# Performance work log

Hardware: AMD Instinct MI355X
Metric: run time of the kernel (lower is better)

The kernel has to match this reference:

```python
import jax, jax.numpy as jnp
import numpy as np

NEG = -1e30  # log-domain 'zero' (safe stand-in for -inf)


def _ctc_loss(logits, labels, label_length, logit_length):
    """Dense-label CTC loss, blank = last class, logits [B,T,C] batch-major.

    Matches tf.nn.ctc_loss(blank_index=-1, logits_time_major=False):
    per-example negative log-likelihood via the standard forward algorithm
    on the blank-extended label sequence of length S = 2L+1.
    """
    B, T, C = logits.shape
    L = labels.shape[1]
    S = 2 * L + 1
    blank = C - 1

    logp = jax.nn.log_softmax(logits, axis=-1)           # [B,T,C]
    lp_t = jnp.moveaxis(logp, 1, 0)                      # [T,B,C]

    # Extended label: blank, l1, blank, l2, ..., blank
    y_ext = jnp.full((B, S), blank, dtype=labels.dtype).at[:, 1::2].set(labels)
    s_idx = jnp.arange(S)
    # s -> s-2 skip allowed iff current symbol is a non-blank differing from s-2
    y_m2 = jnp.pad(y_ext, ((0, 0), (2, 0)), constant_values=blank)[:, :-2]
    skip = (s_idx[None, :] >= 2) & (y_ext != blank) & (y_ext != y_m2)  # [B,S]

    emit0 = jnp.take_along_axis(lp_t[0], y_ext, axis=1)  # [B,S]
    alpha0 = jnp.where(s_idx[None, :] <= 1, emit0, NEG)  # paths start at s=0 or 1

    def step(alpha, lp):
        emit = jnp.take_along_axis(lp, y_ext, axis=1)                      # [B,S]
        a1 = jnp.pad(alpha, ((0, 0), (1, 0)), constant_values=NEG)[:, :-1]  # s-1
        a2 = jnp.pad(alpha, ((0, 0), (2, 0)), constant_values=NEG)[:, :-2]  # s-2
        a2 = jnp.where(skip, a2, NEG)
        new = jnp.logaddexp(jnp.logaddexp(alpha, a1), a2) + emit
        return new, new

    _, alphas = jax.lax.scan(step, alpha0, lp_t[1:])     # [T-1,B,S]
    alphas = jnp.concatenate([alpha0[None], alphas], axis=0)  # [T,B,S]

    b = jnp.arange(B)
    final = alphas[logit_length - 1, b]                  # [B,S] alpha at last frame
    end = 2 * label_length                               # index of final blank
    nll = -jnp.logaddexp(final[b, end], final[b, end - 1])
    return jnp.mean(nll)


def setup_inputs() -> dict:
    key = jax.random.key(0)
    k1, k2, k3 = jax.random.split(key, 3)
    B, T, C, L = 256, 256, 512, 64
    logits = jax.random.normal(k1, (B, T, C), dtype=jnp.float32)
    labels = jax.random.randint(k2, (B, L), 0, C - 1, dtype=jnp.int32)  # never blank
    label_length = jax.random.randint(k3, (B,), 16, L + 1, dtype=jnp.int32)
    logit_length = jnp.full((B,), T, dtype=jnp.int32)
    return {"logits": logits, "labels": labels,
            "label_length": label_length, "logit_length": logit_length}


def reference(logits, labels, label_length, logit_length):
    return _ctc_loss(logits, labels, label_length, logit_length)
```

## Files before the change

kernel.cpp:

```cpp
#include <hip/hip_runtime.h>
#include <math.h>

#define NEGV -1e30f

constexpr int Bc = 256;
constexpr int Tc = 256;
constexpr int Cc = 512;
constexpr int Lc = 64;
constexpr int PW = 8;
constexpr int NROW = Tc / PW;
constexpr int NGRP = Tc / PW;
constexpr float INVLN2 = 1.44269504088896340736f;
constexpr float LN2    = 0.69314718055994530942f;

__device__ __forceinline__ float la2(float a, float b) {
    float m = fmaxf(a, b);
    float d = fabsf(a - b);
    return m + __log2f(exp2f(-d) + 1.0f);
}

__device__ __forceinline__ float lse3(float a, float b, float c) {
    float m = fmaxf(fmaxf(a, b), c);
    return m + __log2f(exp2f(a - m) + exp2f(b - m) + exp2f(c - m));
}

__device__ __forceinline__ float dpp_shr1(float x, float fill) {
    int r = __builtin_amdgcn_update_dpp(__float_as_int(fill), __float_as_int(x),
                                        0x138 , 0xF, 0xF, false);
    return __int_as_float(r);
}

__device__ __forceinline__ float wave_sum_dpp(float v) {
#define DPPADD(ctrl)                                                          \
    v += __int_as_float(__builtin_amdgcn_update_dpp(                          \
        0, __float_as_int(v), (ctrl), 0xF, 0xF, true))
    DPPADD(0x111);
    DPPADD(0x112);
    DPPADD(0x114);
    DPPADD(0x118);
    DPPADD(0x142);
    DPPADD(0x143);
#undef DPPADD
    return __int_as_float(__builtin_amdgcn_readlane(__float_as_int(v), 63));
}

__global__ __launch_bounds__(512) void ctc_k(const float* __restrict__ logits,
                                             const int* __restrict__ labels,
                                             const int* __restrict__ lab_len,
                                             const int* __restrict__ log_len,
                                             float* __restrict__ nll) {
    const int b    = blockIdx.x;
    const int tid  = threadIdx.x;
    const int w    = tid >> 6;
    const int lane = tid & 63;

    __shared__ float em[Tc][66];
    __shared__ float rows[PW][Cc];

    const float* base = logits + (size_t)b * Tc * Cc;
    const int y = labels[b * Lc + lane];

    {
        float* myrow = rows[w];
        const float4* pa = (const float4*)(base + (size_t)w * Cc);
        const float4* pb = (const float4*)(base + (size_t)(w + PW) * Cc);
        const float4* pc = (const float4*)(base + (size_t)(w + 2 * PW) * Cc);
        float4 a0 = pa[lane], a1 = pa[lane + 64];
        float4 b0 = pb[lane], b1 = pb[lane + 64];
        float4 c0 = pc[lane], c1 = pc[lane + 64];

        for (int i = 0; i < NROW; ++i) {
            float4 n0, n1;
            if (i + 3 < NROW) {
                const float4* pn =
                    (const float4*)(base + (size_t)(w + PW * (i + 3)) * Cc);
                n0 = pn[lane]; n1 = pn[lane + 64];
            }
            float e = __expf(a0.x) + __expf(a0.y) + __expf(a0.z) + __expf(a0.w)
                    + __expf(a1.x) + __expf(a1.y) + __expf(a1.z) + __expf(a1.w);
            float lse2 = __log2f(wave_sum_dpp(e));
            ((float4*)myrow)[lane]      = a0;
            ((float4*)myrow)[lane + 64] = a1;
            float xl = myrow[y];
            const int t = w + PW * i;
            em[t][lane] = xl * INVLN2 - lse2;
            if (lane == 63)
                em[t][64] = a1.w * INVLN2 - lse2;
            a0 = b0; a1 = b1;
            b0 = c0; b1 = c1;
            c0 = n0; c1 = n1;
        }
    }
    __syncthreads();
    if (w != 0) return;

    const int  prevlab = __shfl_up(y, 1, 64);
    const bool skip    = (lane >= 1) && (y != prevlab);
    const int  llm1    = log_len[b] - 1;
    float ae = NEGV, ao = NEGV, ax = NEGV;
    float fe = NEGV, fo = NEGV, fx = NEGV;

    auto step = [&](float em_lv, float em_bv, int t) {
        float po = dpp_shr1(ao, NEGV);
        float nae = la2(ae, po) + em_bv;
        float nao = (skip ? lse3(ao, ae, po)
                          : la2(ao, ae)) + em_lv;
        float nax = la2(ax, ao) + em_bv;
        ae = nae; ao = nao; ax = nax;
        if (t == llm1) { fe = ae; fo = ao; fx = ax; }
    };

    for (int g = 0; g < NGRP; ++g) {
        float el[PW], eb[PW];
#pragma unroll
        for (int r = 0; r < PW; ++r) {
            el[r] = em[PW * g + r][lane];
            eb[r] = em[PW * g + r][64];
        }
        if (g == 0) {
            ae = (lane == 0) ? eb[0] : NEGV;
            ao = (lane == 0) ? el[0] : NEGV;
            ax = NEGV;
            if (llm1 == 0) { fe = ae; fo = ao; fx = ax; }
#pragma unroll
            for (int r = 1; r < PW; ++r) step(el[r], eb[r], r);
        } else {
#pragma unroll
            for (int r = 0; r < PW; ++r) step(el[r], eb[r], PW * g + r);
        }
    }

    const int L  = lab_len[b];
    float f0 = (L == Lc) ? __shfl(fx, 63, 64) : __shfl(fe, L, 64);
    float f1 = __shfl(fo, L - 1, 64);
    if (lane == 0) nll[b] = -LN2 * la2(f0, f1);
}

__global__ __launch_bounds__(256) void reduce_k(const float* __restrict__ nll,
                                                float* __restrict__ out) {
    int tid = threadIdx.x;
    float v = nll[tid];
#pragma unroll
    for (int o = 32; o; o >>= 1) v += __shfl_xor(v, o, 64);
    __shared__ float pr[4];
    if ((tid & 63) == 0) pr[tid >> 6] = v;
    __syncthreads();
    if (tid == 0) out[0] = (pr[0] + pr[1] + pr[2] + pr[3]) * (1.0f / Bc);
}

extern "C" void kernel_launch(void* const* d_in, const int* in_sizes, int n_in,
                              void* d_out, int out_size, void* d_ws, size_t ws_size,
                              hipStream_t stream) {
    const float* logits  = (const float*)d_in[0];
    const int*   labels  = (const int*)d_in[1];
    const int*   lab_len = (const int*)d_in[2];
    const int*   log_len = (const int*)d_in[3];
    float* out = (float*)d_out;
    float* nll = (float*)d_ws;

    hipLaunchKernelGGL(ctc_k, dim3(Bc), dim3(512), 0, stream,
                       logits, labels, lab_len, log_len, nll);
    hipLaunchKernelGGL(reduce_k, dim3(1), dim3(256), 0, stream, nll, out);
}
```

Before: 239.9 us.

## Split CTC into a parallel log-sum-exp kernel and a single-wave alpha recursion kernel

Measured after the change: 236.4 us. Within noise of the previous version (-1.4%).

```diff
diff --git a/kernel.cpp b/kernel.cpp
--- a/kernel.cpp
+++ b/kernel.cpp
@@ -7,9 +7,6 @@
 constexpr int Tc = 256;
 constexpr int Cc = 512;
 constexpr int Lc = 64;
-constexpr int PW = 8;
-constexpr int NROW = Tc / PW;
-constexpr int NGRP = Tc / PW;
 constexpr float INVLN2 = 1.44269504088896340736f;
 constexpr float LN2    = 0.69314718055994530942f;
 
@@ -44,55 +41,50 @@
     return __int_as_float(__builtin_amdgcn_readlane(__float_as_int(v), 63));
 }
 
-__global__ __launch_bounds__(512) void ctc_k(const float* __restrict__ logits,
-                                             const int* __restrict__ labels,
-                                             const int* __restrict__ lab_len,
-                                             const int* __restrict__ log_len,
-                                             float* __restrict__ nll) {
+__device__ __forceinline__ float rl(float v, int l) {
+    return __int_as_float(__builtin_amdgcn_readlane(__float_as_int(v), l));
+}
+
+__global__ __launch_bounds__(256) void lse_k(const float* __restrict__ logits,
+                                             float* __restrict__ lse2buf,
+                                             float* __restrict__ embbuf) {
+    const int r    = blockIdx.x * 4 + (threadIdx.x >> 6);
+    const int lane = threadIdx.x & 63;
+
+    const float4* p = (const float4*)(logits + (size_t)r * Cc);
+    float4 a0 = p[lane], a1 = p[lane + 64];
+    float e = __expf(a0.x) + __expf(a0.y) + __expf(a0.z) + __expf(a0.w)
+            + __expf(a1.x) + __expf(a1.y) + __expf(a1.z) + __expf(a1.w);
+    float l2 = __log2f(wave_sum_dpp(e));
+    if (lane == 63) {
+        lse2buf[r] = l2;
+        embbuf[r]  = a1.w * INVLN2 - l2;
+    }
+}
+
+__global__ __launch_bounds__(64) void alpha_k(const float* __restrict__ logits,
+                                              const float* __restrict__ lse2buf,
+                                              const float* __restrict__ embbuf,
+                                              const int* __restrict__ labels,
+                                              const int* __restrict__ lab_len,
+                                              const int* __restrict__ log_len,
+                                              float* __restrict__ nll) {
     const int b    = blockIdx.x;
-    const int tid  = threadIdx.x;
-    const int w    = tid >> 6;
-    const int lane = tid & 63;
-
-    __shared__ float em[Tc][66];
-    __shared__ float rows[PW][Cc];
+    const int lane = threadIdx.x & 63;
 
     const float* base = logits + (size_t)b * Tc * Cc;
     const int y = labels[b * Lc + lane];
 
-    {
-        float* myrow = rows[w];
-        const float4* pa = (const float4*)(base + (size_t)w * Cc);
-        const float4* pb = (const float4*)(base + (size_t)(w + PW) * Cc);
-        const float4* pc = (const float4*)(base + (size_t)(w + 2 * PW) * Cc);
-        float4 a0 = pa[lane], a1 = pa[lane + 64];
-        float4 b0 = pb[lane], b1 = pb[lane + 64];
-        float4 c0 = pc[lane], c1 = pc[lane + 64];
+    float lse_r[4], emb_r[4];
+#pragma unroll
+    for (int q = 0; q < 4; ++q) {
+        lse_r[q] = lse2buf[b * Tc + q * 64 + lane];
+        emb_r[q] = embbuf[b * Tc + q * 64 + lane];
+    }
 
-        for (int i = 0; i < NROW; ++i) {
-            float4 n0, n1;
-            if (i + 3 < NROW) {
-                const float4* pn =
-                    (const float4*)(base + (size_t)(w + PW * (i + 3)) * Cc);
-                n0 = pn[lane]; n1 = pn[lane + 64];
-            }
-            float e = __expf(a0.x) + __expf(a0.y) + __expf(a0.z) + __expf(a0.w)
-                    + __expf(a1.x) + __expf(a1.y) + __expf(a1.z) + __expf(a1.w);
-            float lse2 = __log2f(wave_sum_dpp(e));
-            ((float4*)myrow)[lane]      = a0;
-            ((float4*)myrow)[lane + 64] = a1;
-            float xl = myrow[y];
-            const int t = w + PW * i;
-            em[t][lane] = xl * INVLN2 - lse2;
-            if (lane == 63)
-                em[t][64] = a1.w * INVLN2 - lse2;
-            a0 = b0; a1 = b1;
-            b0 = c0; b1 = c1;
-            c0 = n0; c1 = n1;
-        }
-    }
-    __syncthreads();
-    if (w != 0) return;
+    float g[16];
+#pragma unroll
+    for (int j = 0; j < 16; ++j) g[j] = base[(size_t)j * Cc + y];
 
     const int  prevlab = __shfl_up(y, 1, 64);
     const bool skip    = (lane >= 1) && (y != prevlab);
@@ -110,23 +102,47 @@
         if (t == llm1) { fe = ae; fo = ao; fx = ax; }
     };
 
-    for (int g = 0; g < NGRP; ++g) {
-        float el[PW], eb[PW];
+    {
+        float l2 = rl(lse_r[0], 0);
+        float eb = rl(emb_r[0], 0);
+        float el = g[0] * INVLN2 - l2;
+        g[0] = base[(size_t)16 * Cc + y];
+        ae = (lane == 0) ? eb : NEGV;
+        ao = (lane == 0) ? el : NEGV;
+        ax = NEGV;
+        if (llm1 == 0) { fe = ae; fo = ao; fx = ax; }
 #pragma unroll
-        for (int r = 0; r < PW; ++r) {
-            el[r] = em[PW * g + r][lane];
-            eb[r] = em[PW * g + r][64];
+        for (int j = 1; j < 16; ++j) {
+            float l2j = rl(lse_r[0], j);
+            float ebj = rl(emb_r[0], j);
+            float xg  = g[j];
+            g[j] = base[(size_t)(j + 16) * Cc + y];
+            step(xg * INVLN2 - l2j, ebj, j);
         }
-        if (g == 0) {
-            ae = (lane == 0) ? eb[0] : NEGV;
-            ao = (lane == 0) ? el[0] : NEGV;
-            ax = NEGV;
-            if (llm1 == 0) { fe = ae; fo = ao; fx = ax; }
+    }
+    for (int blk = 1; blk < 4; ++blk) {
 #pragma unroll
-            for (int r = 1; r < PW; ++r) step(el[r], eb[r], r);
-        } else {
+        for (int j = 0; j < 16; ++j) {
+            const int t = blk * 16 + j;
+            float l2j = rl(lse_r[0], t);
+            float ebj = rl(emb_r[0], t);
+            float xg  = g[j];
+            g[j] = base[(size_t)(t + 16) * Cc + y];
+            step(xg * INVLN2 - l2j, ebj, t);
+        }
+    }
 #pragma unroll
-            for (int r = 0; r < PW; ++r) step(el[r], eb[r], PW * g + r);
+    for (int q = 1; q < 4; ++q) {
+        for (int blk = 0; blk < 4; ++blk) {
+#pragma unroll
+            for (int j = 0; j < 16; ++j) {
+                const int t = q * 64 + blk * 16 + j;
+                float l2j = rl(lse_r[q], t & 63);
+                float ebj = rl(emb_r[q], t & 63);
+                float xg  = g[j];
+                if (t + 16 < Tc) g[j] = base[(size_t)(t + 16) * Cc + y];
+                step(xg * INVLN2 - l2j, ebj, t);
+            }
         }
     }
 
@@ -155,10 +171,14 @@
     const int*   labels  = (const int*)d_in[1];
     const int*   lab_len = (const int*)d_in[2];
     const int*   log_len = (const int*)d_in[3];
-    float* out = (float*)d_out;
-    float* nll = (float*)d_ws;
+    float* out     = (float*)d_out;
+    float* nll     = (float*)d_ws;
+    float* lse2buf = (float*)((char*)d_ws + 1024);
+    float* embbuf  = (float*)((char*)d_ws + 1024 + 262144);
 
-    hipLaunchKernelGGL(ctc_k, dim3(Bc), dim3(512), 0, stream,
-                       logits, labels, lab_len, log_len, nll);
+    hipLaunchKernelGGL(lse_k, dim3(Bc * Tc / 4), dim3(256), 0, stream,
+                       logits, lse2buf, embbuf);
+    hipLaunchKernelGGL(alpha_k, dim3(Bc), dim3(64), 0, stream,
+                       logits, lse2buf, embbuf, labels, lab_len, log_len, nll);
     hipLaunchKernelGGL(reduce_k, dim3(1), dim3(256), 0, stream, nll, out);
 }
```
